# Kernel optimization log

Hardware: AMD Instinct MI355X
Metric: run time of the kernel (lower is better)

## Reference

```python
import jax, jax.numpy as jnp
import numpy as np

S_CONST = float(np.log(9.0))   # self.s = log(9)
K = 1.0                        # soft_sign sharpness (config.k)
RHO = 1.0
ALPHA0 = 0.01
BETA0 = 0.1
DECAY = 0.99


def soft_sign(x, k=K):
    # E2Efold soft sign: sigmoid(2*k*x)
    return jax.nn.sigmoid(2.0 * k * x)


def constraint_matrix(x):
    # x: [B, L, 4] -> m: [B, L, L]; pairing constraint AU+CG+UG outer products,
    # symmetrized, with |i-j|<=3 band zeroed (diags mask in torch version).
    base_a, base_u, base_c, base_g = x[..., 0], x[..., 1], x[..., 2], x[..., 3]

    def sym_outer(p, q):
        m = p[:, :, None] * q[:, None, :]
        return m + jnp.swapaxes(m, -1, -2)

    m = sym_outer(base_a, base_u) + sym_outer(base_c, base_g) + sym_outer(base_u, base_g)
    L = x.shape[1]
    i = jnp.arange(L)
    band = jnp.abs(i[:, None] - i[None, :]) <= 3  # [L, L] bool
    return jnp.where(band, jnp.zeros((), m.dtype), m)


def contact_a(a_hat, m):
    a = a_hat * a_hat
    a = (a + jnp.swapaxes(a, -1, -2)) * 0.5
    return a * m


def setup_inputs() -> dict:
    key = jax.random.key(0)
    k1, k2 = jax.random.split(key)
    B, L = 16, 512
    u = jax.random.normal(k1, (B, L, L), jnp.float32) * 2.0
    x = jax.random.uniform(k2, (B, L, 4), jnp.float32)
    return {"u": u, "x": x, "timesteps": 20}


def reference(u, x, timesteps):
    m = constraint_matrix(x)
    u = soft_sign(u - S_CONST) * u
    a_hat = jax.nn.sigmoid(u) * jax.lax.stop_gradient(soft_sign(u - S_CONST))
    a = contact_a(a_hat, m)
    lmbd = jax.lax.stop_gradient(jax.nn.relu(jnp.sum(a, -1) - 1.0))

    # per-step decayed learning rates: step t uses alpha0*decay^t (for grad step)
    # and alpha0*decay^(t+1) for the soft-threshold (torch decays alpha in between)
    t_idx = jnp.arange(timesteps, dtype=jnp.float32)
    alphas = ALPHA0 * DECAY ** t_idx
    betas = BETA0 * DECAY ** t_idx

    def step(carry, ab):
        lmbd, a, a_hat = carry
        alpha, beta = ab
        grad_a = -u / 2.0 + (lmbd * soft_sign(jnp.sum(a, -1) - 1.0))[..., None]
        grad = a_hat * m * (grad_a + jnp.swapaxes(grad_a, -1, -2))
        a_hat_new = a_hat - alpha * grad
        a_hat_new = jax.nn.relu(jnp.abs(a_hat_new) - RHO * alpha * DECAY)
        a_hat_new = jnp.clip(a_hat_new, -1.0, 1.0)
        a_new = contact_a(a_hat_new, m)
        lmbd_new = lmbd + beta * jax.nn.relu(jnp.sum(a_new, -1) - 1.0)
        return (lmbd_new, a_new, a_hat_new), a_new

    _, a_stack = jax.lax.scan(step, (lmbd, a, a_hat), (alphas, betas))
    return a_stack  # [timesteps, B, L, L] == a_t_list[1:]
```

## Files before the change

### kernel.cpp

```cpp
#include <hip/hip_runtime.h>
#include <math.h>

#define BB 16
#define LL 512
#define TS 20
#define TT 64
#define NT (LL / TT)
#define NPAIR (NT * (NT + 1) / 2)
#define NUNIT 32
#define NBLK (BB * NUNIT)
#define BLL (BB * LL * LL)
#define NROW (BB * LL)
#define RSPSTEP (BB * NT * LL)

#define S_CONST 2.19722457733621938f

__device__ __forceinline__ float sgm(float v) { return 1.0f / (1.0f + __expf(-v)); }
__device__ __forceinline__ float ahat_of(float up) {
  return sgm(up) * sgm(2.0f * (up - S_CONST));
}

__device__ __forceinline__ void st_agent(float* p, float v) {
  __hip_atomic_store(p, v, __ATOMIC_RELAXED, __HIP_MEMORY_SCOPE_AGENT);
}
__device__ __forceinline__ float ld_agent(const float* p) {
  return __hip_atomic_load(p, __ATOMIC_RELAXED, __HIP_MEMORY_SCOPE_AGENT);
}

__device__ __forceinline__ void decode_unit(int p, int& RI, int& RJ, bool& dg) {
  if (p < 28) {
    int base = 0, i = 0;
    while (p >= base + (NT - 1 - i)) { base += NT - 1 - i; ++i; }
    RI = i;
    RJ = i + 1 + (p - base);
    dg = false;
  } else {
    int g = p - 28;
    RI = 2 * g;
    RJ = 2 * g + 1;
    dg = true;
  }
}

__global__ __launch_bounds__(256, 2) void k_fused(const float* __restrict__ u,
                                                  const float* __restrict__ x,
                                                  float* __restrict__ rsp,
                                                  float* __restrict__ out) {
  __shared__ float t1[TT][TT + 1];
  __shared__ float t2[TT][TT + 1];
  __shared__ float colp1[16][TT];
  __shared__ float colp2[16][TT];
  __shared__ float rp1[TT];
  __shared__ float rp2[TT];
  __shared__ float xr[2][TT][4];
  __shared__ float xt[2][TT][4];
  __shared__ float cI[TT];
  __shared__ float cJ[TT];

  int b = blockIdx.x / NUNIT;
  int p = blockIdx.x % NUNIT;
  int RI, RJ;
  bool dg;
  decode_unit(p, RI, RJ, dg);
  int C1 = dg ? RI : RJ;
  int C2 = dg ? RJ : RI;

  int tid = threadIdx.x;
  int tx = tid & 15, ty = tid >> 4;

  if (tid < 128) {
    int which = tid >> 6;
    int r = tid & 63;
    int gi = (which ? RJ : RI) * TT + r;
    const float* xp = x + ((b * LL) + gi) * 4;
    float A = xp[0], U = xp[1], C = xp[2], G = xp[3];
    xr[which][r][0] = A; xr[which][r][1] = U; xr[which][r][2] = C; xr[which][r][3] = G;
    xt[which][r][0] = U; xt[which][r][1] = A + G; xt[which][r][2] = G; xt[which][r][3] = C + U;
  }

  int lrow = 0;
  if (tid < 128) {
    int which = tid >> 6;
    int r = tid & 63;
    lrow = (which ? RJ : RI) * TT + r;
  }
  float lmbd = 0.0f;

  float av1[4][4], av2[4][4];
  float wv1[4][4], wv2[4][4];
  float mv1[4][4], mv2[4][4];

  __syncthreads();

#pragma unroll
  for (int k = 0; k < 4; ++k) {
    int r = ty + 16 * k;
    {
      int i = RI * TT + r;
      int off = (b * LL + i) * LL + C1 * TT + 4 * tx;
      float4 u4 = *reinterpret_cast<const float4*>(u + off);
      float uu[4] = {u4.x, u4.y, u4.z, u4.w};
#pragma unroll
      for (int q = 0; q < 4; ++q) {
        float up = sgm(2.0f * (uu[q] - S_CONST)) * uu[q];
        t1[r][4 * tx + q] = up;
        av1[k][q] = ahat_of(up);
      }
    }
    {
      int i = RJ * TT + r;
      int off = (b * LL + i) * LL + C2 * TT + 4 * tx;
      float4 u4 = *reinterpret_cast<const float4*>(u + off);
      float uu[4] = {u4.x, u4.y, u4.z, u4.w};
#pragma unroll
      for (int q = 0; q < 4; ++q) {
        float up = sgm(2.0f * (uu[q] - S_CONST)) * uu[q];
        t2[r][4 * tx + q] = up;
        av2[k][q] = ahat_of(up);
      }
    }
  }
  __syncthreads();

  {
    float (*T1)[TT + 1] = dg ? t1 : t2;
    float (*T2)[TT + 1] = dg ? t2 : t1;
    float (*xc1)[4] = dg ? xt[0] : xt[1];
    float (*xc2)[4] = dg ? xt[1] : xt[0];
    float* rsp0 = rsp;

#pragma unroll
    for (int k = 0; k < 4; ++k) {
      int r = ty + 16 * k;
      {
        int i = RI * TT + r;
        float rs = 0.0f;
#pragma unroll
        for (int q = 0; q < 4; ++q) {
          int c = 4 * tx + q;
          int j = C1 * TT + c;
          float upT = T1[c][r];
          wv1[k][q] = -0.5f * (t1[r][c] + upT);
          int d = i - j; d = d < 0 ? -d : d;
          float mm = (d <= 3) ? 0.0f
                              : xr[0][r][0] * xc1[c][0] + xr[0][r][1] * xc1[c][1] +
                                    xr[0][r][2] * xc1[c][2] + xr[0][r][3] * xc1[c][3];
          mv1[k][q] = mm;
          float aT = ahat_of(upT);
          float a = av1[k][q];
          rs += 0.5f * (a * a + aT * aT) * mm;
        }
        rs += __shfl_xor(rs, 1); rs += __shfl_xor(rs, 2);
        rs += __shfl_xor(rs, 4); rs += __shfl_xor(rs, 8);
        if (tx == 0) st_agent(&rsp0[(b * NT + C1) * LL + i], rs + 1.0f);
      }
      {
        int i = RJ * TT + r;
        float rs = 0.0f;
#pragma unroll
        for (int q = 0; q < 4; ++q) {
          int c = 4 * tx + q;
          int j = C2 * TT + c;
          float upT = T2[c][r];
          wv2[k][q] = -0.5f * (t2[r][c] + upT);
          int d = i - j; d = d < 0 ? -d : d;
          float mm = (d <= 3) ? 0.0f
                              : xr[1][r][0] * xc2[c][0] + xr[1][r][1] * xc2[c][1] +
                                    xr[1][r][2] * xc2[c][2] + xr[1][r][3] * xc2[c][3];
          mv2[k][q] = mm;
          float aT = ahat_of(upT);
          float a = av2[k][q];
          rs += 0.5f * (a * a + aT * aT) * mm;
        }
        rs += __shfl_xor(rs, 1); rs += __shfl_xor(rs, 2);
        rs += __shfl_xor(rs, 4); rs += __shfl_xor(rs, 8);
        if (tx == 0) st_agent(&rsp0[(b * NT + C2) * LL + i], rs + 1.0f);
      }
    }
  }

  float alpha = 0.01f;
  float beta_prev = 0.0f;

  for (int t = 0; t < TS; ++t) {
    if (tid < 128) {
      const float* rp = rsp + (size_t)t * RSPSTEP + b * NT * LL + lrow;
      float v0, v1, v2, v3, v4, v5, v6, v7;
      for (;;) {
        v0 = ld_agent(rp + 0 * LL);
        v1 = ld_agent(rp + 1 * LL);
        v2 = ld_agent(rp + 2 * LL);
        v3 = ld_agent(rp + 3 * LL);
        v4 = ld_agent(rp + 4 * LL);
        v5 = ld_agent(rp + 5 * LL);
        v6 = ld_agent(rp + 6 * LL);
        v7 = ld_agent(rp + 7 * LL);
        bool ok = (v0 != 0.0f) & (v1 != 0.0f) & (v2 != 0.0f) & (v3 != 0.0f) &
                  (v4 != 0.0f) & (v5 != 0.0f) & (v6 != 0.0f) & (v7 != 0.0f);
        if (__all(ok)) break;
        __builtin_amdgcn_s_sleep(2);
        asm volatile("" ::: "memory");
      }
      float rsv = ((v0 + v1) + (v2 + v3)) + ((v4 + v5) + (v6 + v7));
      float dv = rsv - 9.0f;
      float rel = dv > 0.0f ? dv : 0.0f;
      lmbd = (t == 0) ? rel : lmbd + beta_prev * rel;
      float cv = lmbd * sgm(2.0f * dv);
      if (tid >= 64) cJ[tid & 63] = cv; else cI[tid] = cv;
    }
    __syncthreads();

    float thr = alpha * 0.99f;
    float* cc1 = dg ? cI : cJ;
    float* cc2 = dg ? cJ : cI;
    bool last = (t == TS - 1);

    float cp1[4] = {0.f, 0.f, 0.f, 0.f};
    float cp2[4] = {0.f, 0.f, 0.f, 0.f};
#pragma unroll
    for (int k = 0; k < 4; ++k) {
      int r = ty + 16 * k;
      {
        float ci = cI[r];
        float rsv = 0.0f;
#pragma unroll
        for (int q = 0; q < 4; ++q) {
          int c = 4 * tx + q;
          float a = av1[k][q];
          float g = a * mv1[k][q] * (wv1[k][q] + ci + cc1[c]);
          float an = a - alpha * g;
          an = fabsf(an) - thr;
          an = an > 0.0f ? an : 0.0f;
          an = an < 1.0f ? an : 1.0f;
          av1[k][q] = an;
          float v = 0.5f * an * an * mv1[k][q];
          t1[r][c] = v;
          rsv += v;
          cp1[q] += v;
        }
        rsv += __shfl_xor(rsv, 1); rsv += __shfl_xor(rsv, 2);
        rsv += __shfl_xor(rsv, 4); rsv += __shfl_xor(rsv, 8);
        if (tx == 0) rp1[r] = rsv;
      }
      {
        float ci = cJ[r];
        float rsv = 0.0f;
#pragma unroll
        for (int q = 0; q < 4; ++q) {
          int c = 4 * tx + q;
          float a = av2[k][q];
          float g = a * mv2[k][q] * (wv2[k][q] + ci + cc2[c]);
          float an = a - alpha * g;
          an = fabsf(an) - thr;
          an = an > 0.0f ? an : 0.0f;
          an = an < 1.0f ? an : 1.0f;
          av2[k][q] = an;
          float v = 0.5f * an * an * mv2[k][q];
          t2[r][c] = v;
          rsv += v;
          cp2[q] += v;
        }
        rsv += __shfl_xor(rsv, 1); rsv += __shfl_xor(rsv, 2);
        rsv += __shfl_xor(rsv, 4); rsv += __shfl_xor(rsv, 8);
        if (tx == 0) rp2[r] = rsv;
      }
    }
#pragma unroll
    for (int q = 0; q < 4; ++q) {
      colp1[ty][4 * tx + q] = cp1[q];
      colp2[ty][4 * tx + q] = cp2[q];
    }
    __syncthreads();

    if (!last) {
      float* rs_next = rsp + (size_t)(t + 1) * RSPSTEP;
      if (tid < 64) {
        int i = tid;
        float vsum = rp1[i];
        float (*cpA)[TT] = dg ? colp1 : colp2;
#pragma unroll
        for (int y = 0; y < 16; ++y) vsum += cpA[y][i];
        st_agent(&rs_next[(b * NT + C1) * LL + RI * TT + i], vsum + 1.0f);
      } else if (tid < 128) {
        int i = tid - 64;
        float vsum = rp2[i];
        float (*cpB)[TT] = dg ? colp2 : colp1;
#pragma unroll
        for (int y = 0; y < 16; ++y) vsum += cpB[y][i];
        st_agent(&rs_next[(b * NT + C2) * LL + RJ * TT + i], vsum + 1.0f);
      }
    }

    float (*T1)[TT + 1] = dg ? t1 : t2;
    float (*T2)[TT + 1] = dg ? t2 : t1;
    float* op = out + (size_t)t * BLL;
#pragma unroll
    for (int k = 0; k < 4; ++k) {
      int r = ty + 16 * k;
      {
        int i = RI * TT + r;
        int off = (b * LL + i) * LL + C1 * TT + 4 * tx;
        float res[4];
#pragma unroll
        for (int q = 0; q < 4; ++q) {
          int c = 4 * tx + q;
          float a = av1[k][q];
          res[q] = 0.5f * a * a * mv1[k][q] + T1[c][r];
        }
        *reinterpret_cast<float4*>(op + off) = make_float4(res[0], res[1], res[2], res[3]);
      }
      {
        int i = RJ * TT + r;
        int off = (b * LL + i) * LL + C2 * TT + 4 * tx;
        float res[4];
#pragma unroll
        for (int q = 0; q < 4; ++q) {
          int c = 4 * tx + q;
          float a = av2[k][q];
          res[q] = 0.5f * a * a * mv2[k][q] + T2[c][r];
        }
        *reinterpret_cast<float4*>(op + off) = make_float4(res[0], res[1], res[2], res[3]);
      }
    }

    beta_prev = (t == 0) ? 0.1f : beta_prev * 0.99f;
    alpha *= 0.99f;
  }
}

__device__ __forceinline__ void decode_pair(int p, int& I, int& J) {
  int base = 0, i = 0;
  while (p >= base + (NT - i)) { base += NT - i; ++i; }
  I = i;
  J = i + (p - base);
}

__global__ __launch_bounds__(256) void k_init(const float* __restrict__ u,
                                              const float* __restrict__ x,
                                              float* __restrict__ w,
                                              float* __restrict__ ah,
                                              float* __restrict__ rowsum) {
  __shared__ float up1[TT][TT + 1];
  __shared__ float up2[TT][TT + 1];
  __shared__ float xr[2][TT][4];
  __shared__ float xt[2][TT][4];

  int b = blockIdx.x / NPAIR;
  int p = blockIdx.x % NPAIR;
  int I, J;
  decode_pair(p, I, J);
  bool diag = (I == J);
  int tid = threadIdx.x;
  int tx = tid & 15, ty = tid >> 4;

  if (tid < 128) {
    int which = tid >> 6;
    int r = tid & 63;
    int gi = (which ? J : I) * TT + r;
    const float* xp = x + ((b * LL) + gi) * 4;
    float A = xp[0], U = xp[1], C = xp[2], G = xp[3];
    xr[which][r][0] = A; xr[which][r][1] = U; xr[which][r][2] = C; xr[which][r][3] = G;
    xt[which][r][0] = U; xt[which][r][1] = A + G; xt[which][r][2] = G; xt[which][r][3] = C + U;
  }

  float a1r[4][4], a2r[4][4];

#pragma unroll
  for (int k = 0; k < 4; ++k) {
    int r = ty + 16 * k;
    {
      int i = I * TT + r;
      int off = (b * LL + i) * LL + J * TT + 4 * tx;
      float4 u4 = *reinterpret_cast<const float4*>(u + off);
      float uu[4] = {u4.x, u4.y, u4.z, u4.w};
      float av[4];
#pragma unroll
      for (int q = 0; q < 4; ++q) {
        float up = sgm(2.0f * (uu[q] - S_CONST)) * uu[q];
        up1[r][4 * tx + q] = up;
        av[q] = ahat_of(up);
        a1r[k][q] = av[q];
      }
      *reinterpret_cast<float4*>(ah + off) = make_float4(av[0], av[1], av[2], av[3]);
    }
    if (!diag) {
      int i = J * TT + r;
      int off = (b * LL + i) * LL + I * TT + 4 * tx;
      float4 u4 = *reinterpret_cast<const float4*>(u + off);
      float uu[4] = {u4.x, u4.y, u4.z, u4.w};
      float av[4];
#pragma unroll
      for (int q = 0; q < 4; ++q) {
        float up = sgm(2.0f * (uu[q] - S_CONST)) * uu[q];
        up2[r][4 * tx + q] = up;
        av[q] = ahat_of(up);
        a2r[k][q] = av[q];
      }
      *reinterpret_cast<float4*>(ah + off) = make_float4(av[0], av[1], av[2], av[3]);
    }
  }
  __syncthreads();

  float (*U2)[TT + 1] = diag ? up1 : up2;

#pragma unroll
  for (int k = 0; k < 4; ++k) {
    int r = ty + 16 * k;
    {
      int i = I * TT + r;
      int off = (b * LL + i) * LL + J * TT + 4 * tx;
      float wv[4];
      float rs = 0.0f;
#pragma unroll
      for (int q = 0; q < 4; ++q) {
        int c = 4 * tx + q;
        int j = J * TT + c;
        float upT = U2[c][r];
        wv[q] = -0.5f * (up1[r][c] + upT);
        int d = i - j; d = d < 0 ? -d : d;
        float mm = (d <= 3) ? 0.0f
                            : xr[0][r][0] * xt[1][c][0] + xr[0][r][1] * xt[1][c][1] +
                                  xr[0][r][2] * xt[1][c][2] + xr[0][r][3] * xt[1][c][3];
        float aT = ahat_of(upT);
        float a = a1r[k][q];
        rs += 0.5f * (a * a + aT * aT) * mm;
      }
      *reinterpret_cast<float4*>(w + off) = make_float4(wv[0], wv[1], wv[2], wv[3]);
      rs += __shfl_xor(rs, 1); rs += __shfl_xor(rs, 2);
      rs += __shfl_xor(rs, 4); rs += __shfl_xor(rs, 8);
      if (tx == 0) atomicAdd(&rowsum[b * LL + i], rs);
    }
    if (!diag) {
      int i = J * TT + r;
      int off = (b * LL + i) * LL + I * TT + 4 * tx;
      float wv[4];
      float rs = 0.0f;
#pragma unroll
      for (int q = 0; q < 4; ++q) {
        int c = 4 * tx + q;
        int j = I * TT + c;
        float upT = up1[c][r];
        wv[q] = -0.5f * (up2[r][c] + upT);
        int d = i - j; d = d < 0 ? -d : d;
        float mm = (d <= 3) ? 0.0f
                            : xr[1][r][0] * xt[0][c][0] + xr[1][r][1] * xt[0][c][1] +
                                  xr[1][r][2] * xt[0][c][2] + xr[1][r][3] * xt[0][c][3];
        float aT = ahat_of(upT);
        float a = a2r[k][q];
        rs += 0.5f * (a * a + aT * aT) * mm;
      }
      *reinterpret_cast<float4*>(w + off) = make_float4(wv[0], wv[1], wv[2], wv[3]);
      rs += __shfl_xor(rs, 1); rs += __shfl_xor(rs, 2);
      rs += __shfl_xor(rs, 4); rs += __shfl_xor(rs, 8);
      if (tx == 0) atomicAdd(&rowsum[b * LL + i], rs);
    }
  }
}

__global__ __launch_bounds__(256) void k_c(float* __restrict__ lmbd,
                                           const float* __restrict__ rs,
                                           float* __restrict__ cc,
                                           float* __restrict__ rsn,
                                           float beta_prev, int first) {
  int idx = blockIdx.x * blockDim.x + threadIdx.x;
  if (idx >= NROW) return;
  float t = rs[idx] - 1.0f;
  float rel = t > 0.0f ? t : 0.0f;
  float l = first ? rel : lmbd[idx] + beta_prev * rel;
  lmbd[idx] = l;
  cc[idx] = l * sgm(2.0f * t);
  rsn[idx] = 0.0f;
}

__global__ __launch_bounds__(256) void k_step(const float* __restrict__ x,
                                              const float* __restrict__ w,
                                              float* __restrict__ ah,
                                              const float* __restrict__ cvec,
                                              float* __restrict__ rsn,
                                              float* __restrict__ out,
                                              float alpha, float thr) {
  __shared__ float an1[TT][TT + 1];
  __shared__ float an2[TT][TT + 1];
  __shared__ float xr[2][TT][4];
  __shared__ float xt[2][TT][4];
  __shared__ float cI[TT];
  __shared__ float cJ[TT];

  int b = blockIdx.x / NPAIR;
  int p = blockIdx.x % NPAIR;
  int I, J;
  decode_pair(p, I, J);
  bool diag = (I == J);
  int tid = threadIdx.x;
  int tx = tid & 15, ty = tid >> 4;

  if (tid < 128) {
    int which = tid >> 6;
    int r = tid & 63;
    int gi = (which ? J : I) * TT + r;
    const float* xp = x + ((b * LL) + gi) * 4;
    float A = xp[0], U = xp[1], C = xp[2], G = xp[3];
    xr[which][r][0] = A; xr[which][r][1] = U; xr[which][r][2] = C; xr[which][r][3] = G;
    xt[which][r][0] = U; xt[which][r][1] = A + G; xt[which][r][2] = G; xt[which][r][3] = C + U;
  } else {
    int t2i = tid - 128;
    int which = t2i >> 6;
    int r = t2i & 63;
    int gi = (which ? J : I) * TT + r;
    float cv = cvec[b * LL + gi];
    if (which) cJ[r] = cv; else cI[r] = cv;
  }
  __syncthreads();

  float m1[4][4], m2[4][4];

#pragma unroll
  for (int k = 0; k < 4; ++k) {
    int r = ty + 16 * k;
    {
      int i = I * TT + r;
      int off = (b * LL + i) * LL + J * TT + 4 * tx;
      float4 a4 = *reinterpret_cast<const float4*>(ah + off);
      float4 w4 = *reinterpret_cast<const float4*>(w + off);
      float av[4] = {a4.x, a4.y, a4.z, a4.w};
      float wv[4] = {w4.x, w4.y, w4.z, w4.w};
      float ci = cI[r];
      float res[4];
#pragma unroll
      for (int q = 0; q < 4; ++q) {
        int c = 4 * tx + q;
        int j = J * TT + c;
        int d = i - j; d = d < 0 ? -d : d;
        float mm = (d <= 3) ? 0.0f
                            : xr[0][r][0] * xt[1][c][0] + xr[0][r][1] * xt[1][c][1] +
                                  xr[0][r][2] * xt[1][c][2] + xr[0][r][3] * xt[1][c][3];
        m1[k][q] = mm;
        float g = av[q] * mm * (wv[q] + ci + cJ[c]);
        float an = av[q] - alpha * g;
        an = fabsf(an) - thr;
        an = an > 0.0f ? an : 0.0f;
        an = an < 1.0f ? an : 1.0f;
        res[q] = an;
        an1[r][c] = an;
      }
      *reinterpret_cast<float4*>(ah + off) = make_float4(res[0], res[1], res[2], res[3]);
    }
    if (!diag) {
      int i = J * TT + r;
      int off = (b * LL + i) * LL + I * TT + 4 * tx;
      float4 a4 = *reinterpret_cast<const float4*>(ah + off);
      float4 w4 = *reinterpret_cast<const float4*>(w + off);
      float av[4] = {a4.x, a4.y, a4.z, a4.w};
      float wv[4] = {w4.x, w4.y, w4.z, w4.w};
      float ci = cJ[r];
      float res[4];
#pragma unroll
      for (int q = 0; q < 4; ++q) {
        int c = 4 * tx + q;
        int j = I * TT + c;
        int d = i - j; d = d < 0 ? -d : d;
        float mm = (d <= 3) ? 0.0f
                            : xr[1][r][0] * xt[0][c][0] + xr[1][r][1] * xt[0][c][1] +
                                  xr[1][r][2] * xt[0][c][2] + xr[1][r][3] * xt[0][c][3];
        m2[k][q] = mm;
        float g = av[q] * mm * (wv[q] + ci + cI[c]);
        float an = av[q] - alpha * g;
        an = fabsf(an) - thr;
        an = an > 0.0f ? an : 0.0f;
        an = an < 1.0f ? an : 1.0f;
        res[q] = an;
        an2[r][c] = an;
      }
      *reinterpret_cast<float4*>(ah + off) = make_float4(res[0], res[1], res[2], res[3]);
    }
  }
  __syncthreads();

  float (*A2)[TT + 1] = diag ? an1 : an2;

#pragma unroll
  for (int k = 0; k < 4; ++k) {
    int r = ty + 16 * k;
    {
      int i = I * TT + r;
      int off = (b * LL + i) * LL + J * TT + 4 * tx;
      float res[4];
      float rs = 0.0f;
#pragma unroll
      for (int q = 0; q < 4; ++q) {
        int c = 4 * tx + q;
        float a = an1[r][c];
        float bt = A2[c][r];
        float v = 0.5f * (a * a + bt * bt) * m1[k][q];
        res[q] = v;
        rs += v;
      }
      *reinterpret_cast<float4*>(out + off) = make_float4(res[0], res[1], res[2], res[3]);
      rs += __shfl_xor(rs, 1); rs += __shfl_xor(rs, 2);
      rs += __shfl_xor(rs, 4); rs += __shfl_xor(rs, 8);
      if (tx == 0) atomicAdd(&rsn[b * LL + i], rs);
    }
    if (!diag) {
      int i = J * TT + r;
      int off = (b * LL + i) * LL + I * TT + 4 * tx;
      float res[4];
      float rs = 0.0f;
#pragma unroll
      for (int q = 0; q < 4; ++q) {
        int c = 4 * tx + q;
        float a = an2[r][c];
        float bt = an1[c][r];
        float v = 0.5f * (a * a + bt * bt) * m2[k][q];
        res[q] = v;
        rs += v;
      }
      *reinterpret_cast<float4*>(out + off) = make_float4(res[0], res[1], res[2], res[3]);
      rs += __shfl_xor(rs, 1); rs += __shfl_xor(rs, 2);
      rs += __shfl_xor(rs, 4); rs += __shfl_xor(rs, 8);
      if (tx == 0) atomicAdd(&rsn[b * LL + i], rs);
    }
  }
}

extern "C" void kernel_launch(void* const* d_in, const int* in_sizes, int n_in,
                              void* d_out, int out_size, void* d_ws, size_t ws_size,
                              hipStream_t stream) {
  const float* u = (const float*)d_in[0];
  const float* x = (const float*)d_in[1];
  float* out = (float*)d_out;
  float* ws = (float*)d_ws;

  float* rsp = ws;
  hipMemsetAsync(rsp, 0, (size_t)TS * RSPSTEP * sizeof(float), stream);

  void* args[] = {(void*)&u, (void*)&x, (void*)&rsp, (void*)&out};
  hipError_t err = hipLaunchCooperativeKernel((void*)k_fused, dim3(NBLK),
                                              dim3(256), args, 0, stream);
  if (err == hipSuccess) return;

  float* w = ws;
  float* ah = ws + (size_t)BLL;
  float* rsA = ws + 2 * (size_t)BLL;
  float* rsB = rsA + NROW;
  float* cc = rsB + NROW;
  float* lmbd = cc + NROW;

  hipMemsetAsync(rsA, 0, NROW * sizeof(float), stream);

  dim3 grid(BB * NPAIR);
  dim3 block(256);
  k_init<<<grid, block, 0, stream>>>(u, x, w, ah, rsA);

  float* ra = rsA;
  float* rb = rsB;
  for (int t = 0; t < TS; ++t) {
    float alpha = 0.01f * powf(0.99f, (float)t);
    float beta_prev = (t > 0) ? 0.1f * powf(0.99f, (float)(t - 1)) : 0.0f;
    k_c<<<dim3((NROW + 255) / 256), block, 0, stream>>>(lmbd, ra, cc, rb, beta_prev,
                                                        t == 0 ? 1 : 0);
    k_step<<<grid, block, 0, stream>>>(x, w, ah, cc, rb, out + (size_t)t * BLL, alpha,
                                       alpha * 0.99f);
    float* tmp = ra; ra = rb; rb = tmp;
  }
}
```

Measured before the change: 407.1 us.

## Defer output stores to idle threads overlapping next step's cross-block spin-wait

The global writes of each step's contact matrix move out of the critical path. Threads 128-255, which previously sat idle while threads 0-127 spin-waited on cross-block row sums, now write the previous step's output from the LDS tiles during that wait, and the last step is written after the loop. The __syncthreads calls are replaced by a barrier that waits only on LDS counters, so the outstanding global stores do not stall it. This relies on the t1/t2 tiles staying unmodified until that barrier, and it uses lighter memory-ordering semantics at the barrier.

```diff
diff --git a/kernel.cpp b/kernel.cpp
--- a/kernel.cpp
+++ b/kernel.cpp
@@ -25,6 +25,12 @@
 }
 __device__ __forceinline__ float ld_agent(const float* p) {
   return __hip_atomic_load(p, __ATOMIC_RELAXED, __HIP_MEMORY_SCOPE_AGENT);
+}
+
+__device__ __forceinline__ void bar_lds() {
+  asm volatile("s_waitcnt lgkmcnt(0)" ::: "memory");
+  __builtin_amdgcn_s_barrier();
+  asm volatile("" ::: "memory");
 }
 
 __device__ __forceinline__ void decode_unit(int p, int& RI, int& RJ, bool& dg) {
@@ -178,6 +184,9 @@
       }
     }
   }
+
+  float (*T1)[TT + 1] = dg ? t1 : t2;
+  float (*T2)[TT + 1] = dg ? t2 : t1;
 
   float alpha = 0.01f;
   float beta_prev = 0.0f;
@@ -207,13 +216,40 @@
       lmbd = (t == 0) ? rel : lmbd + beta_prev * rel;
       float cv = lmbd * sgm(2.0f * dv);
       if (tid >= 64) cJ[tid & 63] = cv; else cI[tid] = cv;
-    }
-    __syncthreads();
+    } else if (t > 0) {
+      int tid2 = tid - 128;
+      int tx2 = tid2 & 15, ty2 = tid2 >> 4;
+      float* op = out + (size_t)(t - 1) * BLL;
+#pragma unroll
+      for (int k = 0; k < 8; ++k) {
+        int r = ty2 + 8 * k;
+        {
+          int off = (b * LL + RI * TT + r) * LL + C1 * TT + 4 * tx2;
+          float res[4];
+#pragma unroll
+          for (int q = 0; q < 4; ++q) {
+            int c = 4 * tx2 + q;
+            res[q] = t1[r][c] + T1[c][r];
+          }
+          *reinterpret_cast<float4*>(op + off) = make_float4(res[0], res[1], res[2], res[3]);
+        }
+        {
+          int off = (b * LL + RJ * TT + r) * LL + C2 * TT + 4 * tx2;
+          float res[4];
+#pragma unroll
+          for (int q = 0; q < 4; ++q) {
+            int c = 4 * tx2 + q;
+            res[q] = t2[r][c] + T2[c][r];
+          }
+          *reinterpret_cast<float4*>(op + off) = make_float4(res[0], res[1], res[2], res[3]);
+        }
+      }
+    }
+    bar_lds();
 
     float thr = alpha * 0.99f;
     float* cc1 = dg ? cI : cJ;
     float* cc2 = dg ? cJ : cI;
-    bool last = (t == TS - 1);
 
     float cp1[4] = {0.f, 0.f, 0.f, 0.f};
     float cp2[4] = {0.f, 0.f, 0.f, 0.f};
@@ -270,9 +306,9 @@
       colp1[ty][4 * tx + q] = cp1[q];
       colp2[ty][4 * tx + q] = cp2[q];
     }
-    __syncthreads();
-
-    if (!last) {
+    bar_lds();
+
+    if (t < TS - 1) {
       float* rs_next = rsp + (size_t)(t + 1) * RSPSTEP;
       if (tid < 64) {
         int i = tid;
@@ -291,40 +327,36 @@
       }
     }
 
-    float (*T1)[TT + 1] = dg ? t1 : t2;
-    float (*T2)[TT + 1] = dg ? t2 : t1;
-    float* op = out + (size_t)t * BLL;
+    beta_prev = (t == 0) ? 0.1f : beta_prev * 0.99f;
+    alpha *= 0.99f;
+  }
+
+  {
+    float* op = out + (size_t)(TS - 1) * BLL;
 #pragma unroll
     for (int k = 0; k < 4; ++k) {
       int r = ty + 16 * k;
       {
-        int i = RI * TT + r;
-        int off = (b * LL + i) * LL + C1 * TT + 4 * tx;
+        int off = (b * LL + RI * TT + r) * LL + C1 * TT + 4 * tx;
         float res[4];
 #pragma unroll
         for (int q = 0; q < 4; ++q) {
           int c = 4 * tx + q;
-          float a = av1[k][q];
-          res[q] = 0.5f * a * a * mv1[k][q] + T1[c][r];
+          res[q] = t1[r][c] + T1[c][r];
         }
         *reinterpret_cast<float4*>(op + off) = make_float4(res[0], res[1], res[2], res[3]);
       }
       {
-        int i = RJ * TT + r;
-        int off = (b * LL + i) * LL + C2 * TT + 4 * tx;
+        int off = (b * LL + RJ * TT + r) * LL + C2 * TT + 4 * tx;
         float res[4];
 #pragma unroll
         for (int q = 0; q < 4; ++q) {
           int c = 4 * tx + q;
-          float a = av2[k][q];
-          res[q] = 0.5f * a * a * mv2[k][q] + T2[c][r];
+          res[q] = t2[r][c] + T2[c][r];
         }
         *reinterpret_cast<float4*>(op + off) = make_float4(res[0], res[1], res[2], res[3]);
       }
     }
-
-    beta_prev = (t == 0) ? 0.1f : beta_prev * 0.99f;
-    alpha *= 0.99f;
   }
 }
 
```

After: 412.8 us. No clear change (+1.4%).
